# Performance work log

Hardware: AMD Instinct MI355X
Metric: run time of the kernel (lower is better)

## Reference

```python
import jax, jax.numpy as jnp
import numpy as np

N = 8_388_608
C = 3  # 3 sentiment classes; |argmax - y| == 2 <=> class-0/class-2 confusion


def setup_inputs() -> dict:
    key = jax.random.key(0)
    k1, k2 = jax.random.split(key)
    logits = jax.random.normal(k1, (N, C), dtype=jnp.float32)
    # original module expects log-softmax outputs
    pre = jax.nn.log_softmax(logits, axis=-1)
    y_true = jax.random.randint(k2, (N,), 0, C, dtype=jnp.int64)
    weight = jnp.float32(2.0)
    return {"pre": pre, "y_true": y_true, "weight": weight}


def reference(pre, y_true, weight):
    # gather log-prob of true class: pre[i, y_true[i]]
    picked = jnp.take_along_axis(pre, y_true[:, None], axis=1)[:, 0]  # [N]
    pred = jnp.argmax(pre, axis=-1)                                   # [N]
    # penalize opposite-polarity mistakes (|pred - y| == 2)
    penal = jnp.abs(pred - y_true) == 2                               # [N] bool
    w = jnp.where(penal, weight, jnp.float32(1.0))                    # [N]
    return -jnp.sum(w * picked) / jnp.float32(pre.shape[0])
```

## Files before the change

### kernel.cpp

```cpp
#include <hip/hip_runtime.h>


#define N_ROWS   8388608
#define BLOCK    256
#define GRID     2048
#define WPB      (BLOCK / 64)
#define NWAVES   (GRID * WPB)
#define ITER     4

__global__ __launch_bounds__(BLOCK) void nll_fused_kernel(
        const float* __restrict__ pre,
        const int*   __restrict__ y_true,
        const float* __restrict__ wptr,
        float*       __restrict__ out) {
    __shared__ float tile[WPB][2][768];
    __shared__ float red[WPB];

    const float wgt  = wptr[0];
    const int   t    = threadIdx.x;
    const int   lane = t & 63;
    const int   wv   = t >> 6;
    const int   W    = (int)blockIdx.x * WPB + wv;

    const float4* __restrict__ pre4 = (const float4*)pre;

    float4 v[ITER][3];
    int    yv[ITER][4];
    #pragma unroll
    for (int k = 0; k < ITER; ++k) {
        const int fb = W * (ITER * 192) + k * 192;
        const int yb = W * (ITER * 256) + k * 256;
        v[k][0] = pre4[fb + lane];
        v[k][1] = pre4[fb +  64 + lane];
        v[k][2] = pre4[fb + 128 + lane];
        yv[k][0] = y_true[yb +        lane];
        yv[k][1] = y_true[yb +  64  + lane];
        yv[k][2] = y_true[yb + 128  + lane];
        yv[k][3] = y_true[yb + 192  + lane];
    }

    float acc = 0.0f;
    #pragma unroll
    for (int k = 0; k < ITER; ++k) {
        float*  slice = tile[wv][k & 1];
        float4* s4    = (float4*)slice;
        s4[lane]       = v[k][0];
        s4[ 64 + lane] = v[k][1];
        s4[128 + lane] = v[k][2];
        asm volatile("s_waitcnt lgkmcnt(0)" ::: "memory");

        #pragma unroll
        for (int m = 0; m < 4; ++m) {
            const int   w0 = 3 * lane + 192 * m;
            const float p0 = slice[w0 + 0];
            const float p1 = slice[w0 + 1];
            const float p2 = slice[w0 + 2];
            const int   tt = yv[k][m];
            const float picked = (tt == 0) ? p0 : ((tt == 1) ? p1 : p2);
            int   pred = 0;
            float mx   = p0;
            if (p1 > mx) { mx = p1; pred = 1; }
            if (p2 > mx) { pred = 2; }
            const bool penal = (pred - tt == 2) || (tt - pred == 2);
            acc += (penal ? wgt : 1.0f) * picked;
        }
    }

    #pragma unroll
    for (int off = 32; off > 0; off >>= 1)
        acc += __shfl_down(acc, off, 64);

    if (lane == 0) red[wv] = acc;
    __syncthreads();

    if (t == 0) {
        const float s = red[0] + red[1] + red[2] + red[3];
        atomicAdd(out, s * (-1.0f / (float)N_ROWS));
    }
}

extern "C" void kernel_launch(void* const* d_in, const int* in_sizes, int n_in,
                              void* d_out, int out_size, void* d_ws, size_t ws_size,
                              hipStream_t stream) {
    const float* pre  = (const float*)d_in[0];
    const int*   y    = (const int*)d_in[1];
    const float* wptr = (const float*)d_in[2];
    float* out = (float*)d_out;

    nll_fused_kernel<<<GRID, BLOCK, 0, stream>>>(pre, y, wptr, out);
}
```

Baseline: 174.2 us.

## Halve grid and software-pipeline loads with a two-deep register prefetch

The grid is halved, so each wave now handles 8 chunks of 256 rows instead of 4 chunks loaded all at once. Loads go through a two-slot register double buffer: while one chunk is staged to LDS and reduced, the chunk two iterations ahead is already being fetched. The goal is to overlap global memory latency with compute while using fewer registers than holding every chunk in flight. The cost is fewer waves in flight and less memory-level parallelism per wave, which could hurt a kernel that is bandwidth-bound.

```diff
diff --git a/kernel.cpp b/kernel.cpp
--- a/kernel.cpp
+++ b/kernel.cpp
@@ -3,10 +3,12 @@
 
 #define N_ROWS   8388608
 #define BLOCK    256
-#define GRID     2048
+#define GRID     1024
 #define WPB      (BLOCK / 64)
 #define NWAVES   (GRID * WPB)
-#define ITER     4
+#define CHUNK    256
+#define NITER    (N_ROWS / (NWAVES * CHUNK))
+#define ROWS_PW  (CHUNK * NITER)
 
 __global__ __launch_bounds__(BLOCK) void nll_fused_kernel(
         const float* __restrict__ pre,
@@ -24,44 +26,66 @@
 
     const float4* __restrict__ pre4 = (const float4*)pre;
 
-    float4 v[ITER][3];
-    int    yv[ITER][4];
+    const int fbW = W * (ROWS_PW * 3 / 4);
+    const int ybW = W * ROWS_PW;
+
+    float4 v[2][3];
+    int    yv[2][4];
+
     #pragma unroll
-    for (int k = 0; k < ITER; ++k) {
-        const int fb = W * (ITER * 192) + k * 192;
-        const int yb = W * (ITER * 256) + k * 256;
-        v[k][0] = pre4[fb + lane];
-        v[k][1] = pre4[fb +  64 + lane];
-        v[k][2] = pre4[fb + 128 + lane];
-        yv[k][0] = y_true[yb +        lane];
-        yv[k][1] = y_true[yb +  64  + lane];
-        yv[k][2] = y_true[yb + 128  + lane];
-        yv[k][3] = y_true[yb + 192  + lane];
+    for (int p = 0; p < 2; ++p) {
+        const int fb = fbW + p * 192;
+        const int yb = ybW + p * 256;
+        v[p][0] = pre4[fb +       lane];
+        v[p][1] = pre4[fb +  64 + lane];
+        v[p][2] = pre4[fb + 128 + lane];
+        yv[p][0] = y_true[yb +       lane];
+        yv[p][1] = y_true[yb +  64 + lane];
+        yv[p][2] = y_true[yb + 128 + lane];
+        yv[p][3] = y_true[yb + 192 + lane];
     }
 
     float acc = 0.0f;
     #pragma unroll
-    for (int k = 0; k < ITER; ++k) {
-        float*  slice = tile[wv][k & 1];
+    for (int k = 0; k < NITER; ++k) {
+        const int b = k & 1;
+        float*  slice = tile[wv][b];
         float4* s4    = (float4*)slice;
-        s4[lane]       = v[k][0];
-        s4[ 64 + lane] = v[k][1];
-        s4[128 + lane] = v[k][2];
+
+        s4[       lane] = v[b][0];
+        s4[ 64 +  lane] = v[b][1];
+        s4[128 +  lane] = v[b][2];
+
+        const int y0 = yv[b][0], y1 = yv[b][1], y2 = yv[b][2], y3 = yv[b][3];
+
+        if (k + 2 < NITER) {
+            const int fb = fbW + (k + 2) * 192;
+            const int yb = ybW + (k + 2) * 256;
+            v[b][0] = pre4[fb +       lane];
+            v[b][1] = pre4[fb +  64 + lane];
+            v[b][2] = pre4[fb + 128 + lane];
+            yv[b][0] = y_true[yb +       lane];
+            yv[b][1] = y_true[yb +  64 + lane];
+            yv[b][2] = y_true[yb + 128 + lane];
+            yv[b][3] = y_true[yb + 192 + lane];
+        }
+
         asm volatile("s_waitcnt lgkmcnt(0)" ::: "memory");
 
+        const int yls[4] = {y0, y1, y2, y3};
         #pragma unroll
         for (int m = 0; m < 4; ++m) {
             const int   w0 = 3 * lane + 192 * m;
             const float p0 = slice[w0 + 0];
             const float p1 = slice[w0 + 1];
             const float p2 = slice[w0 + 2];
-            const int   tt = yv[k][m];
+            const int   tt = yls[m];
             const float picked = (tt == 0) ? p0 : ((tt == 1) ? p1 : p2);
-            int   pred = 0;
-            float mx   = p0;
-            if (p1 > mx) { mx = p1; pred = 1; }
-            if (p2 > mx) { pred = 2; }
-            const bool penal = (pred - tt == 2) || (tt - pred == 2);
+            int   prd = 0;
+            float mx  = p0;
+            if (p1 > mx) { mx = p1; prd = 1; }
+            if (p2 > mx) { prd = 2; }
+            const bool penal = (prd - tt == 2) || (tt - prd == 2);
             acc += (penal ? wgt : 1.0f) * picked;
         }
     }
```

Result: no change. 175.5 us (+0.8%).
